# Performance work log

Hardware: AMD Instinct MI355X
Metric: run time of the kernel (lower is better)

The kernel has to match this reference:

```python
import jax, jax.numpy as jnp
import numpy as np

N, L, D, F, NUM_BAGS = 262144, 1024, 128, 32, 256


def setup_inputs() -> dict:
    key = jax.random.key(0)
    ks = jax.random.split(key, 12)
    x = jax.random.normal(ks[0], (N, L), dtype=jnp.float32)
    idxs = jnp.sort(jax.random.randint(ks[1], (N,), 0, NUM_BAGS, dtype=jnp.int64))
    def lin(k, fan_in, fan_out):
        s = 1.0 / np.sqrt(fan_in)
        return jax.random.uniform(k, (fan_in, fan_out), jnp.float32, -s, s)
    W1 = lin(ks[2], L, D);  b1 = jnp.zeros((D,), jnp.float32)
    Wt = lin(ks[3], D, F);  bt = jnp.zeros((F,), jnp.float32)
    Ws = lin(ks[4], D, F);  bs = jnp.zeros((F,), jnp.float32)
    Wa = lin(ks[5], F, 1);  ba = jnp.zeros((1,), jnp.float32)
    Wp = lin(ks[6], D, F);  bp = jnp.zeros((F,), jnp.float32)
    return {"x": x, "idxs": idxs, "W1": W1, "b1": b1, "Wt": Wt, "bt": bt,
            "Ws": Ws, "bs": bs, "Wa": Wa, "ba": ba, "Wp": Wp, "bp": bp}


def reference(x, idxs, W1, b1, Wt, bt, Ws, bs, Wa, ba, Wp, bp):
    # feature extractor (Dropout is identity at eval time)
    H = jax.nn.relu(x @ W1 + b1)                       # [N, D]
    # gated attention scores
    At = jnp.tanh(H @ Wt + bt)                         # [N, F]
    As = jax.nn.sigmoid(H @ Ws + bs)                   # [N, F]
    a = ((At * As) @ Wa + ba)[:, 0]                    # [N]
    # per-bag (segment) softmax, numerically stable
    amax = jax.ops.segment_max(a, idxs, num_segments=NUM_BAGS)   # [B]
    w = jnp.exp(a - amax[idxs])                         # [N]
    den = jax.ops.segment_sum(w, idxs, num_segments=NUM_BAGS)    # [B]
    w = w / den[idxs]
    # segment weighted reduce: M[b] = sum_i w_i * H_i over bag b
    M = jax.ops.segment_sum(w[:, None] * H, idxs, num_segments=NUM_BAGS)  # [B, D]
    # projector + L2 normalize (torch F.normalize eps=1e-12)
    proj = M @ Wp + bp                                  # [B, F]
    nrm = jnp.maximum(jnp.linalg.norm(proj, axis=1, keepdims=True), 1e-12)
    proj = proj / nrm
    return M, proj
```

## Files before the change

kernel.cpp:

```cpp
#include <hip/hip_runtime.h>
#include <hip/hip_bf16.h>

#define NTOT 262144
#define LDIM 1024
#define DDIM 128
#define FDIM 32
#define NBAGS 256

typedef __attribute__((ext_vector_type(8))) short bf16x8;
typedef __attribute__((ext_vector_type(4))) float f32x4;

__device__ __forceinline__ unsigned short f2b(float f) {
    __hip_bfloat16 h = __float2bfloat16(f);
    return __builtin_bit_cast(unsigned short, h);
}
__device__ __forceinline__ float b2f(unsigned short u) {
    union { float f; unsigned int i; } c;
    c.i = ((unsigned int)u) << 16;
    return c.f;
}

__global__ void k_prep(const float* __restrict__ W1, const float* __restrict__ Wt,
                       const float* __restrict__ Ws,
                       ushort* __restrict__ w1t, ushort* __restrict__ wtT,
                       ushort* __restrict__ wsT,
                       float* __restrict__ Mraw, float* __restrict__ dden) {
    int gid = blockIdx.x * 256 + threadIdx.x;
    if (gid < LDIM * DDIM) {
        int col = gid & 127, k = gid >> 7;
        w1t[col * 1024 + k] = f2b(W1[gid]);
    }
    if (gid < DDIM * FDIM) {
        int f = gid & 31, d = gid >> 5;
        wtT[f * 128 + d] = f2b(Wt[gid]);
        wsT[f * 128 + d] = f2b(Ws[gid]);
    }
    if (gid < NBAGS * DDIM) Mraw[gid] = 0.0f;
    if (gid < NBAGS) dden[gid] = 0.0f;
}

__global__ __launch_bounds__(256, 4) void k_fused_gemm(
    const float* __restrict__ x, const ushort* __restrict__ w1t,
    const ushort* __restrict__ wtT, const ushort* __restrict__ wsT,
    const float* __restrict__ b1,
    const float* __restrict__ bt, const float* __restrict__ bs,
    const float* __restrict__ Wa, const float* __restrict__ ba,
    const int* __restrict__ idxs,
    float* __restrict__ Mraw, float* __restrict__ dden)
{
    __shared__ __align__(16) ushort sAB[16384];
    __shared__ float sb1[128];
    __shared__ float sbt[32], sbs[32], sWa[32];
    __shared__ float sw[128];
    __shared__ int   sbag[128];

    const int t    = threadIdx.x;
    const int lane = t & 63;
    const int wave = t >> 6;
    const int wr   = wave >> 1, wc = wave & 1;
    const int lq   = lane >> 4, lr = lane & 15;
    const int row0 = blockIdx.x * 128;

    if (t < 128) { sb1[t] = b1[t]; sbag[t] = idxs[row0 + t]; }
    if (t < 32)  { sbt[t] = bt[t]; sbs[t] = bs[t]; sWa[t] = Wa[t]; }
    const float ba0 = ba[0];

    f32x4 acc[4][4];
#pragma unroll
    for (int m = 0; m < 4; ++m)
#pragma unroll
        for (int n = 0; n < 4; ++n) acc[m][n] = 0;

    char* sA = (char*)sAB;

    const int arow  = t >> 4;
    const int acol4 = (t & 15) * 4;
    const float* xb = x + (size_t)(row0 + arow) * LDIM + acol4;
    const int a_base = (((acol4 >> 3) ^ (arow & 7)) << 4) + (acol4 & 7) * 2;
    const ushort* wb = w1t + (size_t)(wc * 64 + lr) * 1024;

    float4 av[8];
#pragma unroll
    for (int j = 0; j < 8; ++j) av[j] = *(const float4*)(xb + j * (16 * LDIM));

    for (int kt = 0; kt < 16; ++kt) {
        __syncthreads();

#pragma unroll
        for (int j = 0; j < 8; ++j) {
            float4 f = av[j];
            uint2 pk;
            pk.x = (unsigned)f2b(f.x) | ((unsigned)f2b(f.y) << 16);
            pk.y = (unsigned)f2b(f.z) | ((unsigned)f2b(f.w) << 16);
            *(uint2*)(sA + (arow + 16 * j) * 128 + a_base) = pk;
        }
        __syncthreads();

        if (kt < 15) {
            const float* xk = xb + (kt + 1) * 64;
#pragma unroll
            for (int j = 0; j < 8; ++j) av[j] = *(const float4*)(xk + j * (16 * LDIM));
        }

#pragma unroll
        for (int kk = 0; kk < 2; ++kk) {
            bf16x8 aF[4], bF[4];
#pragma unroll
            for (int m = 0; m < 4; ++m) {
                int ra = wr * 64 + m * 16 + lr;
                aF[m] = *(const bf16x8*)(sA + ra * 128 + (((kk * 4 + lq) ^ (ra & 7)) << 4));
            }
#pragma unroll
            for (int n = 0; n < 4; ++n)
                bF[n] = *(const bf16x8*)(wb + n * 16384 + kt * 64 + kk * 32 + lq * 8);
#pragma unroll
            for (int m = 0; m < 4; ++m)
#pragma unroll
                for (int n = 0; n < 4; ++n)
                    acc[m][n] = __builtin_amdgcn_mfma_f32_16x16x32_bf16(aF[m], bF[n], acc[m][n], 0, 0, 0);
        }
    }
    __syncthreads();

    char* sH = (char*)sAB;
#pragma unroll
    for (int m = 0; m < 4; ++m) {
#pragma unroll
        for (int n = 0; n < 4; ++n) {
            const int colg = wc * 64 + n * 16 + lr;
            const float bias = sb1[colg];
#pragma unroll
            for (int r = 0; r < 4; ++r) {
                const int rowl = wr * 64 + m * 16 + lq * 4 + r;
                float h = acc[m][n][r] + bias;
                h = fmaxf(h, 0.0f);
                *(ushort*)(sH + rowl * 256 + (((colg >> 3) ^ (rowl & 15)) << 4) + (colg & 7) * 2) = f2b(h);
            }
        }
    }
    __syncthreads();

    {
        f32x4 at_[2][2], as_[2][2];
#pragma unroll
        for (int m = 0; m < 2; ++m)
#pragma unroll
            for (int n = 0; n < 2; ++n) { at_[m][n] = 0; as_[m][n] = 0; }

#pragma unroll
        for (int kk = 0; kk < 4; ++kk) {
            bf16x8 aH[2], bT[2], bS[2];
            const int slot = kk * 4 + lq;
#pragma unroll
            for (int m = 0; m < 2; ++m) {
                const int ra = wave * 32 + m * 16 + lr;
                aH[m] = *(const bf16x8*)(sH + ra * 256 + ((slot ^ (ra & 15)) << 4));
            }
#pragma unroll
            for (int n = 0; n < 2; ++n) {
                const int f = n * 16 + lr;
                bT[n] = *(const bf16x8*)(wtT + f * 128 + kk * 32 + lq * 8);
                bS[n] = *(const bf16x8*)(wsT + f * 128 + kk * 32 + lq * 8);
            }
#pragma unroll
            for (int m = 0; m < 2; ++m)
#pragma unroll
                for (int n = 0; n < 2; ++n) {
                    at_[m][n] = __builtin_amdgcn_mfma_f32_16x16x32_bf16(aH[m], bT[n], at_[m][n], 0, 0, 0);
                    as_[m][n] = __builtin_amdgcn_mfma_f32_16x16x32_bf16(aH[m], bS[n], as_[m][n], 0, 0, 0);
                }
        }

#pragma unroll
        for (int m = 0; m < 2; ++m) {
#pragma unroll
            for (int r = 0; r < 4; ++r) {
                float s = 0.f;
#pragma unroll
                for (int n = 0; n < 2; ++n) {
                    const int f = n * 16 + lr;
                    float tv = tanhf(at_[m][n][r] + sbt[f]);
                    float sg = 1.0f / (1.0f + __expf(-(as_[m][n][r] + sbs[f])));
                    s += tv * sg * sWa[f];
                }
                s += __shfl_xor(s, 1);
                s += __shfl_xor(s, 2);
                s += __shfl_xor(s, 4);
                s += __shfl_xor(s, 8);
                if (lr == 0)
                    sw[wave * 32 + m * 16 + lq * 4 + r] = __expf(s + ba0);
            }
        }
    }
    __syncthreads();

    {
        const int d = t & 127, half = t >> 7;
        const int r0 = half * 64;
        float accv = 0.f, accw = 0.f;
        int curbag = sbag[r0];
        for (int r = 0; r < 64; ++r) {
            const int rr = r0 + r;
            const int bg = sbag[rr];
            if (bg != curbag) {
                atomicAdd(&Mraw[curbag * 128 + d], accv);
                if (d == 0) atomicAdd(&dden[curbag], accw);
                accv = 0.f; accw = 0.f; curbag = bg;
            }
            const float w = sw[rr];
            const ushort hv = *(const ushort*)(sH + rr * 256 + ((((d >> 3) ^ (rr & 15))) << 4) + (d & 7) * 2);
            accv += w * b2f(hv);
            accw += w;
        }
        atomicAdd(&Mraw[curbag * 128 + d], accv);
        if (d == 0) atomicAdd(&dden[curbag], accw);
    }
}

__global__ __launch_bounds__(128) void k_final(
    const float* __restrict__ Mraw, const float* __restrict__ dden,
    const float* __restrict__ Wp, const float* __restrict__ bp,
    float* __restrict__ out)
{
    __shared__ float sM[128];
    const int b = blockIdx.x, t = threadIdx.x;
    const float den = dden[b];
    const float inv_den = den > 0.f ? 1.0f / den : 0.0f;

    float m = Mraw[b * 128 + t] * inv_den;
    sM[t] = m;
    out[b * 128 + t] = m;
    __syncthreads();

    if (t < 32) {
        float p = bp[t];
        for (int d = 0; d < 128; ++d) p += sM[d] * Wp[d * 32 + t];
        float ss = p * p;
#pragma unroll
        for (int mm = 1; mm < 32; mm <<= 1) ss += __shfl_xor(ss, mm);
        float nrm = sqrtf(ss);
        out[32768 + b * 32 + t] = p / fmaxf(nrm, 1e-12f);
    }
}

extern "C" void kernel_launch(void* const* d_in, const int* in_sizes, int n_in,
                              void* d_out, int out_size, void* d_ws, size_t ws_size,
                              hipStream_t stream)
{
    const float* x  = (const float*)d_in[0];
    const int*   idxs = (const int*)d_in[1];
    const float* W1 = (const float*)d_in[2];
    const float* b1 = (const float*)d_in[3];
    const float* Wt = (const float*)d_in[4];
    const float* bt = (const float*)d_in[5];
    const float* Ws = (const float*)d_in[6];
    const float* bs = (const float*)d_in[7];
    const float* Wa = (const float*)d_in[8];
    const float* ba = (const float*)d_in[9];
    const float* Wp = (const float*)d_in[10];
    const float* bp = (const float*)d_in[11];
    float* out = (float*)d_out;

    char* ws = (char*)d_ws;
    float*  Mraw = (float*)ws;
    float*  dden = (float*)(ws + 131072);
    ushort* w1t  = (ushort*)(ws + 132096);
    ushort* wtT  = (ushort*)(ws + 132096 + 262144);
    ushort* wsT  = (ushort*)(ws + 132096 + 262144 + 8192);

    k_prep<<<512, 256, 0, stream>>>(W1, Wt, Ws, w1t, wtT, wsT, Mraw, dden);
    k_fused_gemm<<<2048, 256, 0, stream>>>(x, w1t, wtT, wsT, b1, bt, bs, Wa, ba, idxs, Mraw, dden);
    k_final<<<NBAGS, 128, 0, stream>>>(Mraw, dden, Wp, bp, out);
}
```

Before: 269.6 us.

## Stage W1 tiles through double-buffered LDS with 8-wave blocks

Pre-swizzles W1 into per-k-tile bf16 blocks and cooperatively stages each tile into LDS alongside the x tile, replacing per-wave direct global loads of B fragments. Blocks grow to 512 threads with each wave owning a smaller 32x64 output tile, and LDS is double-buffered so one barrier per k-step suffices. This aims to cut redundant global/L2 traffic for weights and barrier overhead, at the cost of larger LDS footprint and reduced per-wave MFMA reuse, which may lower occupancy.

```diff
diff --git a/kernel.cpp b/kernel.cpp
--- a/kernel.cpp
+++ b/kernel.cpp
@@ -22,13 +22,15 @@
 
 __global__ void k_prep(const float* __restrict__ W1, const float* __restrict__ Wt,
                        const float* __restrict__ Ws,
-                       ushort* __restrict__ w1t, ushort* __restrict__ wtT,
+                       ushort* __restrict__ w1t2, ushort* __restrict__ wtT,
                        ushort* __restrict__ wsT,
                        float* __restrict__ Mraw, float* __restrict__ dden) {
     int gid = blockIdx.x * 256 + threadIdx.x;
     if (gid < LDIM * DDIM) {
         int col = gid & 127, k = gid >> 7;
-        w1t[col * 1024 + k] = f2b(W1[gid]);
+        int kt = k >> 6, ko = k & 63;
+        int cc = ko >> 3, kr = ko & 7;
+        w1t2[kt * 8192 + col * 64 + (cc ^ (col & 7)) * 8 + kr] = f2b(W1[gid]);
     }
     if (gid < DDIM * FDIM) {
         int f = gid & 31, d = gid >> 5;
@@ -39,8 +41,8 @@
     if (gid < NBAGS) dden[gid] = 0.0f;
 }
 
-__global__ __launch_bounds__(256, 4) void k_fused_gemm(
-    const float* __restrict__ x, const ushort* __restrict__ w1t,
+__global__ __launch_bounds__(512, 4) void k_fused_gemm(
+    const float* __restrict__ x, const ushort* __restrict__ w1t2,
     const ushort* __restrict__ wtT, const ushort* __restrict__ wsT,
     const float* __restrict__ b1,
     const float* __restrict__ bt, const float* __restrict__ bs,
@@ -48,7 +50,8 @@
     const int* __restrict__ idxs,
     float* __restrict__ Mraw, float* __restrict__ dden)
 {
-    __shared__ __align__(16) ushort sAB[16384];
+    __shared__ __align__(16) ushort sA2[2][8192];
+    __shared__ __align__(16) ushort sB2[2][8192];
     __shared__ float sb1[128];
     __shared__ float sbt[32], sbs[32], sWa[32];
     __shared__ float sw[128];
@@ -65,56 +68,68 @@
     if (t < 32)  { sbt[t] = bt[t]; sbs[t] = bs[t]; sWa[t] = Wa[t]; }
     const float ba0 = ba[0];
 
-    f32x4 acc[4][4];
-#pragma unroll
-    for (int m = 0; m < 4; ++m)
+    f32x4 acc[2][4];
+#pragma unroll
+    for (int m = 0; m < 2; ++m)
 #pragma unroll
         for (int n = 0; n < 4; ++n) acc[m][n] = 0;
-
-    char* sA = (char*)sAB;
 
     const int arow  = t >> 4;
     const int acol4 = (t & 15) * 4;
     const float* xb = x + (size_t)(row0 + arow) * LDIM + acol4;
     const int a_base = (((acol4 >> 3) ^ (arow & 7)) << 4) + (acol4 & 7) * 2;
-    const ushort* wb = w1t + (size_t)(wc * 64 + lr) * 1024;
-
-    float4 av[8];
-#pragma unroll
-    for (int j = 0; j < 8; ++j) av[j] = *(const float4*)(xb + j * (16 * LDIM));
+    const ushort* bb = w1t2 + t * 8;
+
+    float4 av[4];
+    bf16x8 bv[2];
+#pragma unroll
+    for (int j = 0; j < 4; ++j) av[j] = *(const float4*)(xb + j * (32 * LDIM));
+#pragma unroll
+    for (int jj = 0; jj < 2; ++jj) bv[jj] = *(const bf16x8*)(bb + jj * 4096);
 
     for (int kt = 0; kt < 16; ++kt) {
-        __syncthreads();
-
-#pragma unroll
-        for (int j = 0; j < 8; ++j) {
+        const int p = kt & 1;
+        char* sA = (char*)sA2[p];
+        char* sB = (char*)sB2[p];
+
+#pragma unroll
+        for (int j = 0; j < 4; ++j) {
             float4 f = av[j];
             uint2 pk;
             pk.x = (unsigned)f2b(f.x) | ((unsigned)f2b(f.y) << 16);
             pk.y = (unsigned)f2b(f.z) | ((unsigned)f2b(f.w) << 16);
-            *(uint2*)(sA + (arow + 16 * j) * 128 + a_base) = pk;
-        }
+            *(uint2*)(sA + (arow + 32 * j) * 128 + a_base) = pk;
+        }
+#pragma unroll
+        for (int jj = 0; jj < 2; ++jj)
+            *(bf16x8*)(sB + t * 16 + jj * 8192) = bv[jj];
+
         __syncthreads();
 
         if (kt < 15) {
             const float* xk = xb + (kt + 1) * 64;
 #pragma unroll
-            for (int j = 0; j < 8; ++j) av[j] = *(const float4*)(xk + j * (16 * LDIM));
+            for (int j = 0; j < 4; ++j) av[j] = *(const float4*)(xk + j * (32 * LDIM));
+            const ushort* bk = bb + (kt + 1) * 8192;
+#pragma unroll
+            for (int jj = 0; jj < 2; ++jj) bv[jj] = *(const bf16x8*)(bk + jj * 4096);
         }
 
 #pragma unroll
         for (int kk = 0; kk < 2; ++kk) {
-            bf16x8 aF[4], bF[4];
-#pragma unroll
-            for (int m = 0; m < 4; ++m) {
-                int ra = wr * 64 + m * 16 + lr;
+            bf16x8 aF[2], bF[4];
+#pragma unroll
+            for (int m = 0; m < 2; ++m) {
+                int ra = wr * 32 + m * 16 + lr;
                 aF[m] = *(const bf16x8*)(sA + ra * 128 + (((kk * 4 + lq) ^ (ra & 7)) << 4));
             }
 #pragma unroll
-            for (int n = 0; n < 4; ++n)
-                bF[n] = *(const bf16x8*)(wb + n * 16384 + kt * 64 + kk * 32 + lq * 8);
-#pragma unroll
-            for (int m = 0; m < 4; ++m)
+            for (int n = 0; n < 4; ++n) {
+                int cb = wc * 64 + n * 16 + lr;
+                bF[n] = *(const bf16x8*)(sB + cb * 128 + (((kk * 4 + lq) ^ (cb & 7)) << 4));
+            }
+#pragma unroll
+            for (int m = 0; m < 2; ++m)
 #pragma unroll
                 for (int n = 0; n < 4; ++n)
                     acc[m][n] = __builtin_amdgcn_mfma_f32_16x16x32_bf16(aF[m], bF[n], acc[m][n], 0, 0, 0);
@@ -122,16 +137,16 @@
     }
     __syncthreads();
 
-    char* sH = (char*)sAB;
-#pragma unroll
-    for (int m = 0; m < 4; ++m) {
+    char* sH = (char*)sA2;
+#pragma unroll
+    for (int m = 0; m < 2; ++m) {
 #pragma unroll
         for (int n = 0; n < 4; ++n) {
             const int colg = wc * 64 + n * 16 + lr;
             const float bias = sb1[colg];
 #pragma unroll
             for (int r = 0; r < 4; ++r) {
-                const int rowl = wr * 64 + m * 16 + lq * 4 + r;
+                const int rowl = wr * 32 + m * 16 + lq * 4 + r;
                 float h = acc[m][n][r] + bias;
                 h = fmaxf(h, 0.0f);
                 *(ushort*)(sH + rowl * 256 + (((colg >> 3) ^ (rowl & 15)) << 4) + (colg & 7) * 2) = f2b(h);
@@ -141,21 +156,16 @@
     __syncthreads();
 
     {
-        f32x4 at_[2][2], as_[2][2];
-#pragma unroll
-        for (int m = 0; m < 2; ++m)
-#pragma unroll
-            for (int n = 0; n < 2; ++n) { at_[m][n] = 0; as_[m][n] = 0; }
+        f32x4 at_[2], as_[2];
+#pragma unroll
+        for (int n = 0; n < 2; ++n) { at_[n] = 0; as_[n] = 0; }
 
 #pragma unroll
         for (int kk = 0; kk < 4; ++kk) {
-            bf16x8 aH[2], bT[2], bS[2];
+            bf16x8 aH, bT[2], bS[2];
             const int slot = kk * 4 + lq;
-#pragma unroll
-            for (int m = 0; m < 2; ++m) {
-                const int ra = wave * 32 + m * 16 + lr;
-                aH[m] = *(const bf16x8*)(sH + ra * 256 + ((slot ^ (ra & 15)) << 4));
-            }
+            const int ra = wave * 16 + lr;
+            aH = *(const bf16x8*)(sH + ra * 256 + ((slot ^ (ra & 15)) << 4));
 #pragma unroll
             for (int n = 0; n < 2; ++n) {
                 const int f = n * 16 + lr;
@@ -163,43 +173,38 @@
                 bS[n] = *(const bf16x8*)(wsT + f * 128 + kk * 32 + lq * 8);
             }
 #pragma unroll
-            for (int m = 0; m < 2; ++m)
-#pragma unroll
-                for (int n = 0; n < 2; ++n) {
-                    at_[m][n] = __builtin_amdgcn_mfma_f32_16x16x32_bf16(aH[m], bT[n], at_[m][n], 0, 0, 0);
-                    as_[m][n] = __builtin_amdgcn_mfma_f32_16x16x32_bf16(aH[m], bS[n], as_[m][n], 0, 0, 0);
-                }
-        }
-
-#pragma unroll
-        for (int m = 0; m < 2; ++m) {
-#pragma unroll
-            for (int r = 0; r < 4; ++r) {
-                float s = 0.f;
-#pragma unroll
-                for (int n = 0; n < 2; ++n) {
-                    const int f = n * 16 + lr;
-                    float tv = tanhf(at_[m][n][r] + sbt[f]);
-                    float sg = 1.0f / (1.0f + __expf(-(as_[m][n][r] + sbs[f])));
-                    s += tv * sg * sWa[f];
-                }
-                s += __shfl_xor(s, 1);
-                s += __shfl_xor(s, 2);
-                s += __shfl_xor(s, 4);
-                s += __shfl_xor(s, 8);
-                if (lr == 0)
-                    sw[wave * 32 + m * 16 + lq * 4 + r] = __expf(s + ba0);
-            }
+            for (int n = 0; n < 2; ++n) {
+                at_[n] = __builtin_amdgcn_mfma_f32_16x16x32_bf16(aH, bT[n], at_[n], 0, 0, 0);
+                as_[n] = __builtin_amdgcn_mfma_f32_16x16x32_bf16(aH, bS[n], as_[n], 0, 0, 0);
+            }
+        }
+
+#pragma unroll
+        for (int r = 0; r < 4; ++r) {
+            float s = 0.f;
+#pragma unroll
+            for (int n = 0; n < 2; ++n) {
+                const int f = n * 16 + lr;
+                float tv = tanhf(at_[n][r] + sbt[f]);
+                float sg = 1.0f / (1.0f + __expf(-(as_[n][r] + sbs[f])));
+                s += tv * sg * sWa[f];
+            }
+            s += __shfl_xor(s, 1);
+            s += __shfl_xor(s, 2);
+            s += __shfl_xor(s, 4);
+            s += __shfl_xor(s, 8);
+            if (lr == 0)
+                sw[wave * 16 + lq * 4 + r] = __expf(s + ba0);
         }
     }
     __syncthreads();
 
     {
-        const int d = t & 127, half = t >> 7;
-        const int r0 = half * 64;
+        const int d = t & 127, q = t >> 7;
+        const int r0 = q * 32;
         float accv = 0.f, accw = 0.f;
         int curbag = sbag[r0];
-        for (int r = 0; r < 64; ++r) {
+        for (int r = 0; r < 32; ++r) {
             const int rr = r0 + r;
             const int bg = sbag[rr];
             if (bg != curbag) {
@@ -264,11 +269,11 @@
     char* ws = (char*)d_ws;
     float*  Mraw = (float*)ws;
     float*  dden = (float*)(ws + 131072);
-    ushort* w1t  = (ushort*)(ws + 132096);
+    ushort* w1t2 = (ushort*)(ws + 132096);
     ushort* wtT  = (ushort*)(ws + 132096 + 262144);
     ushort* wsT  = (ushort*)(ws + 132096 + 262144 + 8192);
 
-    k_prep<<<512, 256, 0, stream>>>(W1, Wt, Ws, w1t, wtT, wsT, Mraw, dden);
-    k_fused_gemm<<<2048, 256, 0, stream>>>(x, w1t, wtT, wsT, b1, bt, bs, Wa, ba, idxs, Mraw, dden);
+    k_prep<<<512, 256, 0, stream>>>(W1, Wt, Ws, w1t2, wtT, wsT, Mraw, dden);
+    k_fused_gemm<<<2048, 512, 0, stream>>>(x, w1t2, wtT, wsT, b1, bt, bs, Wa, ba, idxs, Mraw, dden);
     k_final<<<NBAGS, 128, 0, stream>>>(Mraw, dden, Wp, bp, out);
 }
```

After: 256.4 us. 4.9% less time.
